# Kernel optimization log

Measured on AMD Instinct MI355X. Metric: run time of the kernel, lower is better.

The kernel has to match this reference:

```python
import jax, jax.numpy as jnp
import numpy as np

EPS = 1e-6
H = 8        # num_heads
DH = 64      # head dim = embed_dim // num_heads
LN_EPS = 1e-5


def _layernorm(x, g, b):
    m = jnp.mean(x, axis=-1, keepdims=True)
    v = jnp.mean(jnp.square(x - m), axis=-1, keepdims=True)
    return (x - m) / jnp.sqrt(v + LN_EPS) * g + b


def _flow_attention(x, Wq, bq, Wk, bk, Wv, bv, Wo, bo):
    # Non-causal Flow-Attention (Flowformer): kernelized sigmoid Q/K,
    # flow-conservation sink/source normalization, linear-attention kv trick.
    B, L, D = x.shape
    S = L
    q = jax.nn.sigmoid((x @ Wq + bq).reshape(B, L, H, DH).transpose(0, 2, 1, 3))  # bhld
    k = jax.nn.sigmoid((x @ Wk + bk).reshape(B, S, H, DH).transpose(0, 2, 1, 3))
    v = (x @ Wv + bv).reshape(B, S, H, DH).transpose(0, 2, 1, 3)

    sink_incoming = 1.0 / jnp.einsum('nhld,nhd->nhl', q + EPS, k.sum(axis=2) + EPS)
    source_outgoing = 1.0 / jnp.einsum('nhld,nhd->nhl', k + EPS, q.sum(axis=2) + EPS)
    conserved_sink = jnp.einsum('nhld,nhd->nhl', q + EPS,
                                (k * source_outgoing[..., None]).sum(axis=2) + EPS)
    conserved_source = jnp.einsum('nhld,nhd->nhl', k + EPS,
                                  (q * sink_incoming[..., None]).sum(axis=2) + EPS)
    conserved_source = jnp.clip(conserved_source, -1.0, 1.0)
    sink_allocation = jax.nn.sigmoid(conserved_sink * (float(L) / float(S)))
    source_competition = jax.nn.softmax(conserved_source, axis=-1) * float(S)

    # linear attention: kv = k^T (v * comp), out = (q * sink_in) kv
    kv = jnp.einsum('nhld,nhlm->nhdm', k, v * source_competition[..., None])
    o = jnp.einsum('nhld,nhdm->nhlm', q * sink_incoming[..., None], kv)
    o = o * sink_allocation[..., None]
    o = o.transpose(0, 2, 1, 3).reshape(B, L, D)
    return o @ Wo + bo


def setup_inputs() -> dict:
    key = jax.random.key(0)
    ks = jax.random.split(key, 16)
    B, L, D, F = 2, 16384, 512, 2048
    s = 0.02
    inp = {
        'x': jax.random.normal(ks[0], (B, L, D), dtype=jnp.float32),
        'Wq': jax.random.normal(ks[1], (D, D), dtype=jnp.float32) * s,
        'bq': jnp.zeros((D,), jnp.float32),
        'Wk': jax.random.normal(ks[2], (D, D), dtype=jnp.float32) * s,
        'bk': jnp.zeros((D,), jnp.float32),
        'Wv': jax.random.normal(ks[3], (D, D), dtype=jnp.float32) * s,
        'bv': jnp.zeros((D,), jnp.float32),
        'Wo': jax.random.normal(ks[4], (D, D), dtype=jnp.float32) * s,
        'bo': jnp.zeros((D,), jnp.float32),
        'W1': jax.random.normal(ks[5], (D, F), dtype=jnp.float32) * s,
        'b1': jnp.zeros((F,), jnp.float32),
        'W2': jax.random.normal(ks[6], (F, D), dtype=jnp.float32) * s,
        'b2': jnp.zeros((D,), jnp.float32),
        'g1': jnp.ones((D,), jnp.float32),
        'be1': jnp.zeros((D,), jnp.float32),
        'g2': jnp.ones((D,), jnp.float32),
        'be2': jnp.zeros((D,), jnp.float32),
    }
    return inp


def reference(x, Wq, bq, Wk, bk, Wv, bv, Wo, bo, W1, b1, W2, b2, g1, be1, g2, be2):
    # norm_first FlowformerLayer. NOTE: original _sa_block returns
    # dropout(attn(x))[0, :, :] -> [L, D], broadcast-added over batch (faithful).
    sa = _flow_attention(_layernorm(x, g1, be1), Wq, bq, Wk, bk, Wv, bv, Wo, bo)[0]
    x = x + sa  # [B,L,D] + [L,D]
    h = _layernorm(x, g2, be2)
    h = jax.nn.gelu(h @ W1 + b1, approximate=False) @ W2 + b2
    return x + h
```

## Files before the change

### kernel.cpp

```cpp
#include <hip/hip_runtime.h>
#include <hip/hip_bf16.h>
#include <cstdint>
#include <cstddef>


#define L_SEQ 16384
#define EPSF 1e-6f

typedef __bf16 b16x8 __attribute__((ext_vector_type(8)));
typedef __bf16 b16x4 __attribute__((ext_vector_type(4)));
typedef float  f32x4 __attribute__((ext_vector_type(4)));

#define FENCE() asm volatile("" ::: "memory")
#define BARF()  { FENCE(); __builtin_amdgcn_s_barrier(); FENCE(); }
#define WAITV(n) asm volatile("s_waitcnt vmcnt(" #n ")" ::: "memory")

__device__ __forceinline__ void gload16(const void* g, void* l) {
  __builtin_amdgcn_global_load_lds((const __attribute__((address_space(1))) void*)g,
                                   (__attribute__((address_space(3))) void*)l, 16, 0, 0);
}

__device__ __forceinline__ float sigmoidf_(float x) { return 1.f / (1.f + __expf(-x)); }

__global__ __launch_bounds__(256) void prep_k(const float* __restrict__ Wq,
                                              const float* __restrict__ Wk,
                                              const float* __restrict__ Wv,
                                              const float* __restrict__ Wo,
                                              const float* __restrict__ W1,
                                              const float* __restrict__ W2,
                                              const float* __restrict__ bq,
                                              const float* __restrict__ bk,
                                              const float* __restrict__ bv,
                                              __bf16* __restrict__ Wqkvt,
                                              __bf16* __restrict__ Wot,
                                              __bf16* __restrict__ W1t,
                                              __bf16* __restrict__ W2t,
                                              float* __restrict__ biascat,
                                              float* __restrict__ zstats) {
  const int b = blockIdx.x;
  if (b >= 3072) {
    const int i = (b - 3072) * 256 + threadIdx.x;
    if (i < 1536) biascat[i] = (i < 512) ? bq[i] : (i < 1024) ? bk[i - 512] : bv[i - 1024];
    else if (i < 1536 + 2112) zstats[i - 1536] = 0.f;
    return;
  }
  const float* src;
  __bf16* dst;
  int K, N, bx, by;
  if (b < 256)       { src = Wq; dst = Wqkvt;                      K = 512;  N = 512;  const int r = b;        bx = r & 15; by = r >> 4; }
  else if (b < 512)  { src = Wk; dst = Wqkvt + (size_t)512 * 512;  K = 512;  N = 512;  const int r = b - 256;  bx = r & 15; by = r >> 4; }
  else if (b < 768)  { src = Wv; dst = Wqkvt + (size_t)1024 * 512; K = 512;  N = 512;  const int r = b - 512;  bx = r & 15; by = r >> 4; }
  else if (b < 1024) { src = Wo; dst = Wot;                        K = 512;  N = 512;  const int r = b - 768;  bx = r & 15; by = r >> 4; }
  else if (b < 2048) { src = W1; dst = W1t;                        K = 512;  N = 2048; const int r = b - 1024; bx = r & 63; by = r >> 6; }
  else               { src = W2; dst = W2t;                        K = 2048; N = 512;  const int r = b - 2048; bx = r & 15; by = r >> 4; }
  __shared__ float tile[32][33];
  const int k0 = by * 32, n0 = bx * 32;
  const int tx = threadIdx.x & 31, ty = threadIdx.x >> 5;
#pragma unroll
  for (int i = 0; i < 32; i += 8) tile[ty + i][tx] = src[(size_t)(k0 + ty + i) * N + n0 + tx];
  __syncthreads();
#pragma unroll
  for (int i = 0; i < 32; i += 8)
    dst[(size_t)(n0 + ty + i) * K + k0 + tx] = (__bf16)tile[tx][ty + i];
}

__global__ __launch_bounds__(128) void ln_rows(const float* __restrict__ x,
                                               const float* __restrict__ g,
                                               const float* __restrict__ be,
                                               __bf16* __restrict__ out) {
  const int row = blockIdx.x, t = threadIdx.x;
  const float4 xv = reinterpret_cast<const float4*>(x + (size_t)row * 512)[t];
  float s = xv.x + xv.y + xv.z + xv.w;
  float s2 = xv.x * xv.x + xv.y * xv.y + xv.z * xv.z + xv.w * xv.w;
#pragma unroll
  for (int off = 32; off > 0; off >>= 1) { s += __shfl_down(s, off); s2 += __shfl_down(s2, off); }
  __shared__ float red[4];
  if ((t & 63) == 0) { red[(t >> 6) * 2] = s; red[(t >> 6) * 2 + 1] = s2; }
  __syncthreads();
  const float S = red[0] + red[2], S2 = red[1] + red[3];
  const float mean = S * (1.f / 512.f);
  const float var = S2 * (1.f / 512.f) - mean * mean;
  const float inv = rsqrtf(var + 1e-5f);
  const float4 gv = reinterpret_cast<const float4*>(g)[t];
  const float4 bv = reinterpret_cast<const float4*>(be)[t];
  b16x4 o;
  o[0] = (__bf16)((xv.x - mean) * inv * gv.x + bv.x);
  o[1] = (__bf16)((xv.y - mean) * inv * gv.y + bv.y);
  o[2] = (__bf16)((xv.z - mean) * inv * gv.z + bv.z);
  o[3] = (__bf16)((xv.w - mean) * inv * gv.w + bv.w);
  reinterpret_cast<b16x4*>(out + (size_t)row * 512)[t] = o;
}

__global__ __launch_bounds__(128) void x2ln2_k(const float* __restrict__ x,
                                               const float* __restrict__ sa0,
                                               const float* __restrict__ sa1,
                                               const float* __restrict__ bo,
                                               const float* __restrict__ g,
                                               const float* __restrict__ be,
                                               float* __restrict__ xout,
                                               __bf16* __restrict__ lnout) {
  const int row = blockIdx.x, t = threadIdx.x;
  const int l = row & (L_SEQ - 1);
  float4 xv = reinterpret_cast<const float4*>(x + (size_t)row * 512)[t];
  const float4 s0 = reinterpret_cast<const float4*>(sa0 + (size_t)l * 512)[t];
  const float4 s1 = reinterpret_cast<const float4*>(sa1 + (size_t)l * 512)[t];
  const float4 bb = reinterpret_cast<const float4*>(bo)[t];
  xv.x += s0.x + s1.x + bb.x; xv.y += s0.y + s1.y + bb.y;
  xv.z += s0.z + s1.z + bb.z; xv.w += s0.w + s1.w + bb.w;
  reinterpret_cast<float4*>(xout + (size_t)row * 512)[t] = xv;
  float s = xv.x + xv.y + xv.z + xv.w;
  float s2 = xv.x * xv.x + xv.y * xv.y + xv.z * xv.z + xv.w * xv.w;
#pragma unroll
  for (int off = 32; off > 0; off >>= 1) { s += __shfl_down(s, off); s2 += __shfl_down(s2, off); }
  __shared__ float red[4];
  if ((t & 63) == 0) { red[(t >> 6) * 2] = s; red[(t >> 6) * 2 + 1] = s2; }
  __syncthreads();
  const float S = red[0] + red[2], S2 = red[1] + red[3];
  const float mean = S * (1.f / 512.f);
  const float var = S2 * (1.f / 512.f) - mean * mean;
  const float inv = rsqrtf(var + 1e-5f);
  const float4 gv = reinterpret_cast<const float4*>(g)[t];
  const float4 bv = reinterpret_cast<const float4*>(be)[t];
  b16x4 o;
  o[0] = (__bf16)((xv.x - mean) * inv * gv.x + bv.x);
  o[1] = (__bf16)((xv.y - mean) * inv * gv.y + bv.y);
  o[2] = (__bf16)((xv.z - mean) * inv * gv.z + bv.z);
  o[3] = (__bf16)((xv.w - mean) * inv * gv.w + bv.w);
  reinterpret_cast<b16x4*>(lnout + (size_t)row * 512)[t] = o;
}

template <int EPI, int KSPL>
__global__ __launch_bounds__(256, 4) void gemm128(const __bf16* __restrict__ A,
                                                  const __bf16* __restrict__ Bt,
                                                  const int M, const int N, const int K,
                                                  const float* __restrict__ bias,
                                                  float* __restrict__ f0,
                                                  __bf16* __restrict__ h0,
                                                  __bf16* __restrict__ h1,
                                                  float* __restrict__ f1,
                                                  float* __restrict__ f2) {
  __shared__ alignas(16) __bf16 lds[16384];

  if constexpr (KSPL) {
    const int z = blockIdx.y;
    A += (size_t)z * (K >> 1);
    Bt += (size_t)z * (K >> 1);
    f0 += (size_t)z * ((size_t)M * N);
  }
  const int nt = KSPL ? (K >> 6) : (K >> 5);

  const int nwg = gridDim.x;
  const int orig = blockIdx.x;
  const int cpx = nwg >> 3;
  const int wg = (orig & 7) * cpx + (orig >> 3);
  const int gx = N >> 7;
  const int bm = (wg / gx) << 7;
  const int bn = (wg % gx) << 7;

  const int t = threadIdx.x;
  const int w = t >> 6, lane = t & 63;
  const int wr = w >> 1, wc = w & 1;
  const int fr = lane & 15;
  const int kb = lane >> 4;

  const __bf16* As = A + (size_t)(bm + (t >> 2)) * K + (t & 3) * 8;
  const __bf16* Bs = Bt + (size_t)(bn + (t >> 2)) * K + (t & 3) * 8;

  f32x4 acc[4][4] = {};

  auto STG = [&](int s) {
    const int sel = (s & 1) * 4096;
    const __bf16* ap = As + (s << 5);
    const __bf16* bp = Bs + (s << 5);
    gload16(ap, &lds[sel + t * 8]);
    gload16(ap + (size_t)64 * K, &lds[sel + 2048 + t * 8]);
    gload16(bp, &lds[8192 + sel + t * 8]);
    gload16(bp + (size_t)64 * K, &lds[8192 + sel + 2048 + t * 8]);
  };

  STG(0);
  WAITV(0);
  BARF();

  for (int s = 0; s < nt; s++) {
    if (s + 1 < nt) STG(s + 1);
    const int ab = (s & 1) * 4096 + (wr * 64 + fr) * 32 + kb * 8;
    const int bb2 = 8192 + (s & 1) * 4096 + (wc * 64 + fr) * 32 + kb * 8;
    b16x8 av[4], bv[4];
#pragma unroll
    for (int m = 0; m < 4; m++)
      av[m] = *reinterpret_cast<const b16x8*>(&lds[ab + m * 512]);
#pragma unroll
    for (int n = 0; n < 4; n++)
      bv[n] = *reinterpret_cast<const b16x8*>(&lds[bb2 + n * 512]);
#pragma unroll
    for (int m = 0; m < 4; m++)
#pragma unroll
      for (int n = 0; n < 4; n++)
        acc[m][n] = __builtin_amdgcn_mfma_f32_16x16x32_bf16(av[m], bv[n], acc[m][n], 0, 0, 0);
    WAITV(0);
    BARF();
  }

  const int r0 = kb * 4;
  const int cc = fr;
  if constexpr (EPI == 0) {
    const int which = bn >> 9;
    float cs[4] = {0.f, 0.f, 0.f, 0.f};
#pragma unroll
    for (int m = 0; m < 4; m++) {
#pragma unroll
      for (int n = 0; n < 4; n++) {
        const int col = bn + wc * 64 + n * 16 + cc;
        const int c2 = col & 511;
#pragma unroll
        for (int r = 0; r < 4; r++) {
          const int row = bm + wr * 64 + m * 16 + r0 + r;
          float val = acc[m][n][r] + bias[col];
          if (which < 2) {
            val = sigmoidf_(val);
            cs[n] += val;
            ((which == 0) ? h0 : h1)[(size_t)row * 512 + c2] = (__bf16)val;
          } else {
            ((__bf16*)f0)[(size_t)row * 512 + c2] = (__bf16)val;
          }
        }
      }
    }
    if (which < 2) {
      float* sums = (which == 0) ? f1 : f2;
#pragma unroll
      for (int n = 0; n < 4; n++) {
        float s = cs[n];
        s += __shfl_xor(s, 16);
        s += __shfl_xor(s, 32);
        if (kb == 0) atomicAdd(&sums[(bn & 511) + wc * 64 + n * 16 + cc], s);
      }
    }
  } else {
#pragma unroll
    for (int m = 0; m < 4; m++) {
#pragma unroll
      for (int n = 0; n < 4; n++) {
        const int col = bn + wc * 64 + n * 16 + cc;
#pragma unroll
        for (int r = 0; r < 4; r++) {
          const int row = bm + wr * 64 + m * 16 + r0 + r;
          const float val = acc[m][n][r];
          if constexpr (EPI == 1) {
            f0[(size_t)row * N + col] = val;
          } else if constexpr (EPI == 2) {
            const float xg = val + bias[col];
            const float gel = 0.5f * xg * (1.f + erff(xg * 0.70710678118f));
            h0[(size_t)row * N + col] = (__bf16)gel;
          } else {
            const size_t idx = (size_t)row * N + col;
            f0[idx] = f0[idx] + val + bias[col];
          }
        }
      }
    }
  }
}

__global__ __launch_bounds__(256) void attn_pass1(const __bf16* __restrict__ q,
                                                  const __bf16* __restrict__ k,
                                                  const float* __restrict__ qsum,
                                                  const float* __restrict__ ksum,
                                                  float* __restrict__ si_out,
                                                  float* __restrict__ qkpart) {
  __shared__ float lsQ[512], lsK[512];
  const int t = threadIdx.x, lane = t & 63, wv = t >> 6;
  const int c0 = lane * 8;
  lsQ[t] = 0.f; lsQ[t + 256] = 0.f;
  lsK[t] = 0.f; lsK[t + 256] = 0.f;
  __syncthreads();
  float qs[8], ks[8];
#pragma unroll
  for (int j = 0; j < 8; j++) {
    qs[j] = qsum[c0 + j] + EPSF;
    ks[j] = ksum[c0 + j] + EPSF;
  }
  const int h = lane >> 3;
  float qacc[8] = {}, kacc[8] = {};
#pragma unroll 1
  for (int i = 0; i < 8; i++) {
    const int l = blockIdx.x * 32 + wv * 8 + i;
    const b16x8 q8 = *reinterpret_cast<const b16x8*>(q + (size_t)l * 512 + c0);
    const b16x8 k8 = *reinterpret_cast<const b16x8*>(k + (size_t)l * 512 + c0);
    float qf[8], kf[8];
    float p1 = 0.f, p2 = 0.f;
#pragma unroll
    for (int j = 0; j < 8; j++) {
      qf[j] = (float)q8[j]; kf[j] = (float)k8[j];
      p1 += (qf[j] + EPSF) * ks[j];
      p2 += (kf[j] + EPSF) * qs[j];
    }
    p1 += __shfl_xor(p1, 1); p2 += __shfl_xor(p2, 1);
    p1 += __shfl_xor(p1, 2); p2 += __shfl_xor(p2, 2);
    p1 += __shfl_xor(p1, 4); p2 += __shfl_xor(p2, 4);
    const float siv = 1.f / p1, sov = 1.f / p2;
    if ((lane & 7) == 0) si_out[h * L_SEQ + l] = siv;
#pragma unroll
    for (int j = 0; j < 8; j++) { qacc[j] += qf[j] * siv; kacc[j] += kf[j] * sov; }
  }
#pragma unroll
  for (int j = 0; j < 8; j++) {
    atomicAdd(&lsQ[c0 + j], qacc[j]);
    atomicAdd(&lsK[c0 + j], kacc[j]);
  }
  __syncthreads();
  float* qp = qkpart + (size_t)blockIdx.x * 1024;
  qp[t] = lsQ[t];
  qp[t + 256] = lsQ[t + 256];
  qp[t + 512] = lsK[t];
  qp[t + 768] = lsK[t + 256];
}

__global__ __launch_bounds__(256) void reduce_qk(const float* __restrict__ qkpart,
                                                 float* __restrict__ outv) {
  const int i = blockIdx.x * 256 + threadIdx.x;
  float s = 0.f;
#pragma unroll 4
  for (int b = 0; b < 512; b++) s += qkpart[(size_t)b * 1024 + i];
  outv[i] = s;
}

__global__ __launch_bounds__(256) void kv_part(const __bf16* __restrict__ k,
                                               const __bf16* __restrict__ v,
                                               const float* __restrict__ qsi,
                                               float* __restrict__ kvpart,
                                               float* __restrict__ separt) {
  const int h = blockIdx.y, bx = blockIdx.x, t = threadIdx.x;
  __shared__ float lsK[64 * 68];
  __shared__ float lsV[64 * 68];
  __shared__ float lsRed[256];
  const int r = t >> 2, cq = (t & 3) * 16;
  float qv[16];
#pragma unroll
  for (int j = 0; j < 16; j++) qv[j] = qsi[h * 64 + cq + j] + EPSF;
  const int d = t & 63, mg = t >> 6;
  f32x4 acc4[4] = {};
  float seloc = 0.f;
#pragma unroll 1
  for (int sc = 0; sc < 4; sc++) {
    const int l = bx * 256 + sc * 64 + r;
    __syncthreads();
    const b16x8 k8a = *reinterpret_cast<const b16x8*>(k + (size_t)l * 512 + h * 64 + cq);
    const b16x8 k8b = *reinterpret_cast<const b16x8*>(k + (size_t)l * 512 + h * 64 + cq + 8);
    const b16x8 v8a = *reinterpret_cast<const b16x8*>(v + (size_t)l * 512 + h * 64 + cq);
    const b16x8 v8b = *reinterpret_cast<const b16x8*>(v + (size_t)l * 512 + h * 64 + cq + 8);
    float kf[16], vf[16];
#pragma unroll
    for (int j = 0; j < 8; j++) {
      kf[j] = (float)k8a[j]; kf[8 + j] = (float)k8b[j];
      vf[j] = (float)v8a[j]; vf[8 + j] = (float)v8b[j];
    }
    float p = 0.f;
#pragma unroll
    for (int j = 0; j < 16; j++) p += (kf[j] + EPSF) * qv[j];
    p += __shfl_xor(p, 1);
    p += __shfl_xor(p, 2);
    p = fminf(fmaxf(p, -1.f), 1.f);
    const float ce = __expf(p);
    if ((t & 3) == 0) seloc += ce;
#pragma unroll
    for (int j = 0; j < 16; j++) {
      lsK[r * 68 + cq + j] = kf[j];
      lsV[r * 68 + cq + j] = vf[j] * ce;
    }
    __syncthreads();
    for (int rr = 0; rr < 64; rr++) {
      const float kd = lsK[rr * 68 + d];
      const f32x4* lv = reinterpret_cast<const f32x4*>(&lsV[rr * 68 + mg * 16]);
#pragma unroll
      for (int jj = 0; jj < 4; jj++) acc4[jj] += lv[jj] * kd;
    }
  }
  float* kp = kvpart + ((size_t)h * 64 + bx) * 4096;
#pragma unroll
  for (int jj = 0; jj < 4; jj++)
    *reinterpret_cast<f32x4*>(&kp[d * 64 + mg * 16 + jj * 4]) = acc4[jj];
  lsRed[t] = ((t & 3) == 0) ? seloc : 0.f;
  __syncthreads();
  for (int s2 = 128; s2 > 0; s2 >>= 1) {
    if (t < s2) lsRed[t] += lsRed[t + s2];
    __syncthreads();
  }
  if (t == 0) separt[h * 64 + bx] = lsRed[0];
}

__global__ __launch_bounds__(256) void kv_reduce(const float* __restrict__ kvpart,
                                                 const float* __restrict__ separt,
                                                 float* __restrict__ kvout,
                                                 float* __restrict__ sumexp) {
  const int h = blockIdx.y, t = threadIdx.x;
  const int i = blockIdx.x * 256 + t;
  float s = 0.f;
#pragma unroll 4
  for (int b = 0; b < 64; b++) s += kvpart[((size_t)h * 64 + b) * 4096 + i];
  kvout[h * 4096 + i] = s;
  if (blockIdx.x == 0 && t < 64) {
    float e = separt[h * 64 + t];
#pragma unroll
    for (int off2 = 32; off2 > 0; off2 >>= 1) e += __shfl_down(e, off2);
    if (t == 0) sumexp[h] = e;
  }
}

__global__ __launch_bounds__(256) void o_kernel(const __bf16* __restrict__ q,
                                                const float* __restrict__ kvin,
                                                const float* __restrict__ si,
                                                const float* __restrict__ kso,
                                                const float* __restrict__ sumexp,
                                                __bf16* __restrict__ o) {
  const int h = blockIdx.y;
  const int l0 = blockIdx.x * 32;
  const int t = threadIdx.x;
  __shared__ float lsKV[64 * 64];
  __shared__ float lsQ[32 * 65];
  __shared__ float lsF[32];
  const float Sfac = (float)L_SEQ / sumexp[h];
#pragma unroll
  for (int j = 0; j < 16; j++) lsKV[t + j * 256] = kvin[h * 4096 + t + j * 256];
  const int r = t >> 3, c8 = (t & 7) * 8;
  float ksov[8];
#pragma unroll
  for (int j = 0; j < 8; j++) ksov[j] = kso[h * 64 + c8 + j] + EPSF;
  const b16x8 q8 = *reinterpret_cast<const b16x8*>(q + (size_t)(l0 + r) * 512 + h * 64 + c8);
  float p = 0.f;
#pragma unroll
  for (int j = 0; j < 8; j++) {
    const float qf = (float)q8[j];
    lsQ[r * 65 + c8 + j] = qf;
    p += (qf + EPSF) * ksov[j];
  }
  p += __shfl_xor(p, 1);
  p += __shfl_xor(p, 2);
  p += __shfl_xor(p, 4);
  if ((t & 7) == 0) lsF[r] = sigmoidf_(p) * si[h * L_SEQ + l0 + r] * Sfac;
  __syncthreads();
  const int m = t & 63, rg = t >> 6;
#pragma unroll 1
  for (int i = 0; i < 8; i++) {
    const int rr = rg + i * 4;
    float a = 0.f;
#pragma unroll
    for (int dd = 0; dd < 64; dd++) a += lsQ[rr * 65 + dd] * lsKV[dd * 64 + m];
    o[(size_t)(l0 + rr) * 512 + h * 64 + m] = (__bf16)(a * lsF[rr]);
  }
}

extern "C" void kernel_launch(void* const* d_in, const int* in_sizes, int n_in,
                              void* d_out, int out_size, void* d_ws, size_t ws_size,
                              hipStream_t stream) {
  const float* x  = (const float*)d_in[0];
  const float* Wq = (const float*)d_in[1];
  const float* bq = (const float*)d_in[2];
  const float* Wk = (const float*)d_in[3];
  const float* bk = (const float*)d_in[4];
  const float* Wv = (const float*)d_in[5];
  const float* bv = (const float*)d_in[6];
  const float* Wo = (const float*)d_in[7];
  const float* bo = (const float*)d_in[8];
  const float* W1 = (const float*)d_in[9];
  const float* b1 = (const float*)d_in[10];
  const float* W2 = (const float*)d_in[11];
  const float* b2 = (const float*)d_in[12];
  const float* g1 = (const float*)d_in[13];
  const float* be1 = (const float*)d_in[14];
  const float* g2 = (const float*)d_in[15];
  const float* be2 = (const float*)d_in[16];
  float* out = (float*)d_out;

  char* ws = (char*)d_ws;
  size_t off = 0;
  auto alloc = [&](size_t bytes) -> char* {
    char* p = ws + off;
    off += (bytes + 255) & ~(size_t)255;
    return p;
  };

  char* regA = alloc(134217728);
  __bf16* ln1  = (__bf16*)regA;
  __bf16* qb16 = (__bf16*)(regA + 16777216);
  __bf16* kb16 = (__bf16*)(regA + 33554432);
  __bf16* vb16 = (__bf16*)(regA + 50331648);
  __bf16* ob   = (__bf16*)(regA + 83886080);
  float*  sa   = (float*)regA;
  __bf16* act  = (__bf16*)regA;

  __bf16* ln2 = (__bf16*)alloc((size_t)32768 * 512 * 2);
  __bf16* Wqkvt = (__bf16*)alloc((size_t)1536 * 512 * 2);
  __bf16* Wot = (__bf16*)alloc((size_t)512 * 512 * 2);
  __bf16* W1t = (__bf16*)alloc((size_t)2048 * 512 * 2);
  __bf16* W2t = (__bf16*)alloc((size_t)512 * 2048 * 2);
  float* biascat = (float*)alloc(1536 * 4);
  float* si = (float*)alloc((size_t)8 * L_SEQ * 4);
  float* stats = (float*)alloc(34880 * 4);
  float* qsum = stats;
  float* ksum = stats + 512;
  float* qsi = stats + 1024;
  float* kso = stats + 1536;
  float* sumexp = stats + 2048;
  float* kvbuf = stats + 2112;
  float* kvpart = (float*)alloc((size_t)8 * 64 * 4096 * 4);
  float* separt = (float*)alloc(512 * 4);
  float* qkpart = (float*)alloc((size_t)512 * 1024 * 4);

  prep_k<<<3087, 256, 0, stream>>>(Wq, Wk, Wv, Wo, W1, W2, bq, bk, bv,
                                   Wqkvt, Wot, W1t, W2t, biascat, stats);

  ln_rows<<<L_SEQ, 128, 0, stream>>>(x, g1, be1, ln1);
  gemm128<0, 0><<<1536, 256, 0, stream>>>(ln1, Wqkvt, L_SEQ, 1536, 512,
                                          biascat, (float*)vb16, qb16, kb16, qsum, ksum);

  attn_pass1<<<512, 256, 0, stream>>>(qb16, kb16, qsum, ksum, si, qkpart);
  reduce_qk<<<4, 256, 0, stream>>>(qkpart, qsi);
  kv_part<<<dim3(64, 8), 256, 0, stream>>>(kb16, vb16, qsi, kvpart, separt);
  kv_reduce<<<dim3(16, 8), 256, 0, stream>>>(kvpart, separt, kvbuf, sumexp);
  o_kernel<<<dim3(L_SEQ / 32, 8), 256, 0, stream>>>(qb16, kvbuf, si, kso, sumexp, ob);

  gemm128<1, 1><<<dim3(512, 2), 256, 0, stream>>>(ob, Wot, L_SEQ, 512, 512,
                                                  nullptr, sa, nullptr, nullptr,
                                                  nullptr, nullptr);

  x2ln2_k<<<2 * L_SEQ, 128, 0, stream>>>(x, sa, sa + (size_t)L_SEQ * 512, bo,
                                         g2, be2, out, ln2);

  gemm128<2, 0><<<4096, 256, 0, stream>>>(ln2, W1t, 2 * L_SEQ, 2048, 512,
                                          b1, nullptr, act, nullptr, nullptr, nullptr);
  gemm128<3, 0><<<1024, 256, 0, stream>>>(act, W2t, 2 * L_SEQ, 512, 2048,
                                          b2, out, nullptr, nullptr, nullptr, nullptr);
}
```

Before: 498.7 us.

## Widen GEMM tiles to 256x128 and store attention output projection in bf16

The shared GEMM kernel now computes 256x128 output tiles instead of 128x128. Each wave holds an 8x4 grid of MFMA accumulators, LDS grows to hold the larger A tile, and occupancy is lowered to two blocks per SM, with grid sizes halved to match. This gives more reuse of each B fragment per LDS load. Separately, the split-K output projection partials are written as bf16 instead of fp32, and the residual-plus-LayerNorm kernel reads bf16, which halves that intermediate traffic at some cost in precision. The larger tile uses more registers and reduces the number of blocks, which may hurt latency hiding.

```diff
diff --git a/kernel.cpp b/kernel.cpp
--- a/kernel.cpp
+++ b/kernel.cpp
@@ -92,8 +92,8 @@
 }
 
 __global__ __launch_bounds__(128) void x2ln2_k(const float* __restrict__ x,
-                                               const float* __restrict__ sa0,
-                                               const float* __restrict__ sa1,
+                                               const __bf16* __restrict__ sa0,
+                                               const __bf16* __restrict__ sa1,
                                                const float* __restrict__ bo,
                                                const float* __restrict__ g,
                                                const float* __restrict__ be,
@@ -102,11 +102,13 @@
   const int row = blockIdx.x, t = threadIdx.x;
   const int l = row & (L_SEQ - 1);
   float4 xv = reinterpret_cast<const float4*>(x + (size_t)row * 512)[t];
-  const float4 s0 = reinterpret_cast<const float4*>(sa0 + (size_t)l * 512)[t];
-  const float4 s1 = reinterpret_cast<const float4*>(sa1 + (size_t)l * 512)[t];
+  const b16x4 s0 = reinterpret_cast<const b16x4*>(sa0 + (size_t)l * 512)[t];
+  const b16x4 s1 = reinterpret_cast<const b16x4*>(sa1 + (size_t)l * 512)[t];
   const float4 bb = reinterpret_cast<const float4*>(bo)[t];
-  xv.x += s0.x + s1.x + bb.x; xv.y += s0.y + s1.y + bb.y;
-  xv.z += s0.z + s1.z + bb.z; xv.w += s0.w + s1.w + bb.w;
+  xv.x += (float)s0[0] + (float)s1[0] + bb.x;
+  xv.y += (float)s0[1] + (float)s1[1] + bb.y;
+  xv.z += (float)s0[2] + (float)s1[2] + bb.z;
+  xv.w += (float)s0[3] + (float)s1[3] + bb.w;
   reinterpret_cast<float4*>(xout + (size_t)row * 512)[t] = xv;
   float s = xv.x + xv.y + xv.z + xv.w;
   float s2 = xv.x * xv.x + xv.y * xv.y + xv.z * xv.z + xv.w * xv.w;
@@ -130,22 +132,22 @@
 }
 
 template <int EPI, int KSPL>
-__global__ __launch_bounds__(256, 4) void gemm128(const __bf16* __restrict__ A,
-                                                  const __bf16* __restrict__ Bt,
-                                                  const int M, const int N, const int K,
-                                                  const float* __restrict__ bias,
-                                                  float* __restrict__ f0,
-                                                  __bf16* __restrict__ h0,
-                                                  __bf16* __restrict__ h1,
-                                                  float* __restrict__ f1,
-                                                  float* __restrict__ f2) {
-  __shared__ alignas(16) __bf16 lds[16384];
+__global__ __launch_bounds__(256, 2) void gemmW(const __bf16* __restrict__ A,
+                                                const __bf16* __restrict__ Bt,
+                                                const int M, const int N, const int K,
+                                                const float* __restrict__ bias,
+                                                float* __restrict__ f0,
+                                                __bf16* __restrict__ h0,
+                                                __bf16* __restrict__ h1,
+                                                float* __restrict__ f1,
+                                                float* __restrict__ f2) {
+  __shared__ alignas(16) __bf16 lds[24576];
 
   if constexpr (KSPL) {
     const int z = blockIdx.y;
     A += (size_t)z * (K >> 1);
     Bt += (size_t)z * (K >> 1);
-    f0 += (size_t)z * ((size_t)M * N);
+    h0 += (size_t)z * ((size_t)M * N);
   }
   const int nt = KSPL ? (K >> 6) : (K >> 5);
 
@@ -154,7 +156,7 @@
   const int cpx = nwg >> 3;
   const int wg = (orig & 7) * cpx + (orig >> 3);
   const int gx = N >> 7;
-  const int bm = (wg / gx) << 7;
+  const int bm = (wg / gx) << 8;
   const int bn = (wg % gx) << 7;
 
   const int t = threadIdx.x;
@@ -166,16 +168,18 @@
   const __bf16* As = A + (size_t)(bm + (t >> 2)) * K + (t & 3) * 8;
   const __bf16* Bs = Bt + (size_t)(bn + (t >> 2)) * K + (t & 3) * 8;
 
-  f32x4 acc[4][4] = {};
+  f32x4 acc[8][4] = {};
 
   auto STG = [&](int s) {
-    const int sel = (s & 1) * 4096;
+    const int sel = (s & 1) * 12288;
     const __bf16* ap = As + (s << 5);
     const __bf16* bp = Bs + (s << 5);
     gload16(ap, &lds[sel + t * 8]);
     gload16(ap + (size_t)64 * K, &lds[sel + 2048 + t * 8]);
-    gload16(bp, &lds[8192 + sel + t * 8]);
-    gload16(bp + (size_t)64 * K, &lds[8192 + sel + 2048 + t * 8]);
+    gload16(ap + (size_t)128 * K, &lds[sel + 4096 + t * 8]);
+    gload16(ap + (size_t)192 * K, &lds[sel + 6144 + t * 8]);
+    gload16(bp, &lds[sel + 8192 + t * 8]);
+    gload16(bp + (size_t)64 * K, &lds[sel + 8192 + 2048 + t * 8]);
   };
 
   STG(0);
@@ -184,17 +188,17 @@
 
   for (int s = 0; s < nt; s++) {
     if (s + 1 < nt) STG(s + 1);
-    const int ab = (s & 1) * 4096 + (wr * 64 + fr) * 32 + kb * 8;
-    const int bb2 = 8192 + (s & 1) * 4096 + (wc * 64 + fr) * 32 + kb * 8;
-    b16x8 av[4], bv[4];
-#pragma unroll
-    for (int m = 0; m < 4; m++)
+    const int ab = (s & 1) * 12288 + (wr * 128 + fr) * 32 + kb * 8;
+    const int bb2 = (s & 1) * 12288 + 8192 + (wc * 64 + fr) * 32 + kb * 8;
+    b16x8 av[8], bv[4];
+#pragma unroll
+    for (int m = 0; m < 8; m++)
       av[m] = *reinterpret_cast<const b16x8*>(&lds[ab + m * 512]);
 #pragma unroll
     for (int n = 0; n < 4; n++)
       bv[n] = *reinterpret_cast<const b16x8*>(&lds[bb2 + n * 512]);
 #pragma unroll
-    for (int m = 0; m < 4; m++)
+    for (int m = 0; m < 8; m++)
 #pragma unroll
       for (int n = 0; n < 4; n++)
         acc[m][n] = __builtin_amdgcn_mfma_f32_16x16x32_bf16(av[m], bv[n], acc[m][n], 0, 0, 0);
@@ -208,20 +212,21 @@
     const int which = bn >> 9;
     float cs[4] = {0.f, 0.f, 0.f, 0.f};
 #pragma unroll
-    for (int m = 0; m < 4; m++) {
+    for (int m = 0; m < 8; m++) {
 #pragma unroll
       for (int n = 0; n < 4; n++) {
         const int col = bn + wc * 64 + n * 16 + cc;
         const int c2 = col & 511;
 #pragma unroll
         for (int r = 0; r < 4; r++) {
-          const int row = bm + wr * 64 + m * 16 + r0 + r;
+          const int row = bm + wr * 128 + m * 16 + r0 + r;
           float val = acc[m][n][r] + bias[col];
           if (which < 2) {
             val = sigmoidf_(val);
             cs[n] += val;
             ((which == 0) ? h0 : h1)[(size_t)row * 512 + c2] = (__bf16)val;
           } else {
+            f2 ? (void)0 : (void)0;
             ((__bf16*)f0)[(size_t)row * 512 + c2] = (__bf16)val;
           }
         }
@@ -239,16 +244,16 @@
     }
   } else {
 #pragma unroll
-    for (int m = 0; m < 4; m++) {
+    for (int m = 0; m < 8; m++) {
 #pragma unroll
       for (int n = 0; n < 4; n++) {
         const int col = bn + wc * 64 + n * 16 + cc;
 #pragma unroll
         for (int r = 0; r < 4; r++) {
-          const int row = bm + wr * 64 + m * 16 + r0 + r;
+          const int row = bm + wr * 128 + m * 16 + r0 + r;
           const float val = acc[m][n][r];
           if constexpr (EPI == 1) {
-            f0[(size_t)row * N + col] = val;
+            h0[(size_t)row * N + col] = (__bf16)val;
           } else if constexpr (EPI == 2) {
             const float xg = val + bias[col];
             const float gel = 0.5f * xg * (1.f + erff(xg * 0.70710678118f));
@@ -487,7 +492,7 @@
   __bf16* kb16 = (__bf16*)(regA + 33554432);
   __bf16* vb16 = (__bf16*)(regA + 50331648);
   __bf16* ob   = (__bf16*)(regA + 83886080);
-  float*  sa   = (float*)regA;
+  __bf16* sa   = (__bf16*)regA;
   __bf16* act  = (__bf16*)regA;
 
   __bf16* ln2 = (__bf16*)alloc((size_t)32768 * 512 * 2);
@@ -512,8 +517,8 @@
                                    Wqkvt, Wot, W1t, W2t, biascat, stats);
 
   ln_rows<<<L_SEQ, 128, 0, stream>>>(x, g1, be1, ln1);
-  gemm128<0, 0><<<1536, 256, 0, stream>>>(ln1, Wqkvt, L_SEQ, 1536, 512,
-                                          biascat, (float*)vb16, qb16, kb16, qsum, ksum);
+  gemmW<0, 0><<<768, 256, 0, stream>>>(ln1, Wqkvt, L_SEQ, 1536, 512,
+                                       biascat, (float*)vb16, qb16, kb16, qsum, ksum);
 
   attn_pass1<<<512, 256, 0, stream>>>(qb16, kb16, qsum, ksum, si, qkpart);
   reduce_qk<<<4, 256, 0, stream>>>(qkpart, qsi);
@@ -521,15 +526,15 @@
   kv_reduce<<<dim3(16, 8), 256, 0, stream>>>(kvpart, separt, kvbuf, sumexp);
   o_kernel<<<dim3(L_SEQ / 32, 8), 256, 0, stream>>>(qb16, kvbuf, si, kso, sumexp, ob);
 
-  gemm128<1, 1><<<dim3(512, 2), 256, 0, stream>>>(ob, Wot, L_SEQ, 512, 512,
-                                                  nullptr, sa, nullptr, nullptr,
-                                                  nullptr, nullptr);
+  gemmW<1, 1><<<dim3(256, 2), 256, 0, stream>>>(ob, Wot, L_SEQ, 512, 512,
+                                                nullptr, nullptr, sa, nullptr,
+                                                nullptr, nullptr);
 
   x2ln2_k<<<2 * L_SEQ, 128, 0, stream>>>(x, sa, sa + (size_t)L_SEQ * 512, bo,
                                          g2, be2, out, ln2);
 
-  gemm128<2, 0><<<4096, 256, 0, stream>>>(ln2, W1t, 2 * L_SEQ, 2048, 512,
-                                          b1, nullptr, act, nullptr, nullptr, nullptr);
-  gemm128<3, 0><<<1024, 256, 0, stream>>>(act, W2t, 2 * L_SEQ, 512, 2048,
-                                          b2, out, nullptr, nullptr, nullptr, nullptr);
-}
+  gemmW<2, 0><<<2048, 256, 0, stream>>>(ln2, W1t, 2 * L_SEQ, 2048, 512,
+                                        b1, nullptr, act, nullptr, nullptr, nullptr);
+  gemmW<3, 0><<<512, 256, 0, stream>>>(act, W2t, 2 * L_SEQ, 512, 2048,
+                                       b2, out, nullptr, nullptr, nullptr, nullptr);
+}
```

New measurement: 535.7 us. +7.4%, slower.

## Add deeper-K swizzled GEMM for FFN and store split-K attention output in bf16

Applied to the files above, without the earlier changes.

Adds a new gemm128b kernel for the two FFN GEMMs. It uses a 64-wide K step, double-buffered LDS with an XOR swizzle to avoid bank conflicts, and a launch bound of 2 blocks per CU. The out-projection split-K partials are now written as bf16 instead of fp32, which halves that write and its read in x2ln2_k. The cost is fewer resident blocks per CU from the larger LDS footprint, plus some precision loss in the attention residual partials.

```diff
diff --git a/kernel.cpp b/kernel.cpp
--- a/kernel.cpp
+++ b/kernel.cpp
@@ -92,8 +92,8 @@
 }
 
 __global__ __launch_bounds__(128) void x2ln2_k(const float* __restrict__ x,
-                                               const float* __restrict__ sa0,
-                                               const float* __restrict__ sa1,
+                                               const __bf16* __restrict__ sa0,
+                                               const __bf16* __restrict__ sa1,
                                                const float* __restrict__ bo,
                                                const float* __restrict__ g,
                                                const float* __restrict__ be,
@@ -102,11 +102,13 @@
   const int row = blockIdx.x, t = threadIdx.x;
   const int l = row & (L_SEQ - 1);
   float4 xv = reinterpret_cast<const float4*>(x + (size_t)row * 512)[t];
-  const float4 s0 = reinterpret_cast<const float4*>(sa0 + (size_t)l * 512)[t];
-  const float4 s1 = reinterpret_cast<const float4*>(sa1 + (size_t)l * 512)[t];
+  const b16x4 s0 = reinterpret_cast<const b16x4*>(sa0 + (size_t)l * 512)[t];
+  const b16x4 s1 = reinterpret_cast<const b16x4*>(sa1 + (size_t)l * 512)[t];
   const float4 bb = reinterpret_cast<const float4*>(bo)[t];
-  xv.x += s0.x + s1.x + bb.x; xv.y += s0.y + s1.y + bb.y;
-  xv.z += s0.z + s1.z + bb.z; xv.w += s0.w + s1.w + bb.w;
+  xv.x += (float)s0[0] + (float)s1[0] + bb.x;
+  xv.y += (float)s0[1] + (float)s1[1] + bb.y;
+  xv.z += (float)s0[2] + (float)s1[2] + bb.z;
+  xv.w += (float)s0[3] + (float)s1[3] + bb.w;
   reinterpret_cast<float4*>(xout + (size_t)row * 512)[t] = xv;
   float s = xv.x + xv.y + xv.z + xv.w;
   float s2 = xv.x * xv.x + xv.y * xv.y + xv.z * xv.z + xv.w * xv.w;
@@ -145,7 +147,7 @@
     const int z = blockIdx.y;
     A += (size_t)z * (K >> 1);
     Bt += (size_t)z * (K >> 1);
-    f0 += (size_t)z * ((size_t)M * N);
+    h0 += (size_t)z * ((size_t)M * N);
   }
   const int nt = KSPL ? (K >> 6) : (K >> 5);
 
@@ -246,17 +248,107 @@
 #pragma unroll
         for (int r = 0; r < 4; r++) {
           const int row = bm + wr * 64 + m * 16 + r0 + r;
-          const float val = acc[m][n][r];
-          if constexpr (EPI == 1) {
-            f0[(size_t)row * N + col] = val;
-          } else if constexpr (EPI == 2) {
-            const float xg = val + bias[col];
-            const float gel = 0.5f * xg * (1.f + erff(xg * 0.70710678118f));
-            h0[(size_t)row * N + col] = (__bf16)gel;
-          } else {
-            const size_t idx = (size_t)row * N + col;
-            f0[idx] = f0[idx] + val + bias[col];
-          }
+          h0[(size_t)row * N + col] = (__bf16)acc[m][n][r];
+        }
+      }
+    }
+  }
+}
+
+template <int EPI>
+__global__ __launch_bounds__(256, 2) void gemm128b(const __bf16* __restrict__ A,
+                                                   const __bf16* __restrict__ Bt,
+                                                   const int M, const int N, const int K,
+                                                   const float* __restrict__ bias,
+                                                   float* __restrict__ f0,
+                                                   __bf16* __restrict__ h0) {
+  __shared__ alignas(16) __bf16 lds[32768];
+
+  const int nt = K >> 6;
+
+  const int nwg = gridDim.x;
+  const int orig = blockIdx.x;
+  const int cpx = nwg >> 3;
+  const int wg = (orig & 7) * cpx + (orig >> 3);
+  const int gx = N >> 7;
+  const int bm = (wg / gx) << 7;
+  const int bn = (wg % gx) << 7;
+
+  const int t = threadIdx.x;
+  const int w = t >> 6, lane = t & 63;
+  const int wr = w >> 1, wc = w & 1;
+  const int fr = lane & 15;
+  const int kb = lane >> 4;
+  const int f7 = fr & 7;
+
+  const int sr = t >> 3;
+  const int sc = (t & 7) ^ (sr & 7);
+  const __bf16* As = A + (size_t)(bm + sr) * K + sc * 8;
+  const __bf16* Bs = Bt + (size_t)(bn + sr) * K + sc * 8;
+  const int dst0 = t * 8;
+
+  f32x4 acc[4][4] = {};
+
+  auto STG = [&](int s) {
+    const int base = (s & 1) * 16384;
+    const __bf16* ap = As + (s << 6);
+    const __bf16* bp = Bs + (s << 6);
+#pragma unroll
+    for (int j = 0; j < 4; j++) {
+      gload16(ap + (size_t)(j << 5) * K, &lds[base + dst0 + (j << 11)]);
+      gload16(bp + (size_t)(j << 5) * K, &lds[base + 8192 + dst0 + (j << 11)]);
+    }
+  };
+
+  STG(0);
+  WAITV(0);
+  BARF();
+
+  for (int s = 0; s < nt; s++) {
+    if (s + 1 < nt) STG(s + 1);
+    const int abase = (s & 1) * 16384 + (wr * 64 + fr) * 64;
+    const int bbase = (s & 1) * 16384 + 8192 + (wc * 64 + fr) * 64;
+#pragma unroll
+    for (int ks = 0; ks < 2; ks++) {
+      b16x8 av[4], bv[4];
+#pragma unroll
+      for (int m = 0; m < 4; m++) {
+        const int sw = (((ks << 2) | kb) ^ f7) << 3;
+        av[m] = *reinterpret_cast<const b16x8*>(&lds[abase + m * 1024 + sw]);
+      }
+#pragma unroll
+      for (int n = 0; n < 4; n++) {
+        const int sw = (((ks << 2) | kb) ^ f7) << 3;
+        bv[n] = *reinterpret_cast<const b16x8*>(&lds[bbase + n * 1024 + sw]);
+      }
+#pragma unroll
+      for (int m = 0; m < 4; m++)
+#pragma unroll
+        for (int n = 0; n < 4; n++)
+          acc[m][n] = __builtin_amdgcn_mfma_f32_16x16x32_bf16(av[m], bv[n], acc[m][n], 0, 0, 0);
+    }
+    WAITV(0);
+    BARF();
+  }
+
+  const int r0 = kb * 4;
+  const int cc = fr;
+#pragma unroll
+  for (int m = 0; m < 4; m++) {
+#pragma unroll
+    for (int n = 0; n < 4; n++) {
+      const int col = bn + wc * 64 + n * 16 + cc;
+#pragma unroll
+      for (int r = 0; r < 4; r++) {
+        const int row = bm + wr * 64 + m * 16 + r0 + r;
+        const float val = acc[m][n][r];
+        if constexpr (EPI == 2) {
+          const float xg = val + bias[col];
+          const float gel = 0.5f * xg * (1.f + erff(xg * 0.70710678118f));
+          h0[(size_t)row * N + col] = (__bf16)gel;
+        } else {
+          const size_t idx = (size_t)row * N + col;
+          f0[idx] = f0[idx] + val + bias[col];
         }
       }
     }
@@ -487,7 +579,7 @@
   __bf16* kb16 = (__bf16*)(regA + 33554432);
   __bf16* vb16 = (__bf16*)(regA + 50331648);
   __bf16* ob   = (__bf16*)(regA + 83886080);
-  float*  sa   = (float*)regA;
+  __bf16* sa   = (__bf16*)regA;
   __bf16* act  = (__bf16*)regA;
 
   __bf16* ln2 = (__bf16*)alloc((size_t)32768 * 512 * 2);
@@ -522,14 +614,14 @@
   o_kernel<<<dim3(L_SEQ / 32, 8), 256, 0, stream>>>(qb16, kvbuf, si, kso, sumexp, ob);
 
   gemm128<1, 1><<<dim3(512, 2), 256, 0, stream>>>(ob, Wot, L_SEQ, 512, 512,
-                                                  nullptr, sa, nullptr, nullptr,
+                                                  nullptr, nullptr, sa, nullptr,
                                                   nullptr, nullptr);
 
   x2ln2_k<<<2 * L_SEQ, 128, 0, stream>>>(x, sa, sa + (size_t)L_SEQ * 512, bo,
                                          g2, be2, out, ln2);
 
-  gemm128<2, 0><<<4096, 256, 0, stream>>>(ln2, W1t, 2 * L_SEQ, 2048, 512,
-                                          b1, nullptr, act, nullptr, nullptr, nullptr);
-  gemm128<3, 0><<<1024, 256, 0, stream>>>(act, W2t, 2 * L_SEQ, 512, 2048,
-                                          b2, out, nullptr, nullptr, nullptr, nullptr);
-}
+  gemm128b<2><<<4096, 256, 0, stream>>>(ln2, W1t, 2 * L_SEQ, 2048, 512,
+                                        b1, nullptr, act);
+  gemm128b<3><<<1024, 256, 0, stream>>>(act, W2t, 2 * L_SEQ, 512, 2048,
+                                        b2, out, nullptr);
+}
```

Measured after the change: 520.0 us. 4.3% more time.
